# Kernel optimization log

Hardware: AMD Instinct MI355X
Metric: run time of the kernel (lower is better)

## Reference

```python
import jax, jax.numpy as jnp
import numpy as np

N, M, D = 8192, 8192, 512
TINY = jnp.finfo(jnp.float32).tiny


def setup_inputs() -> dict:
    key = jax.random.key(0)
    k1, k2 = jax.random.split(key)
    x = jax.random.normal(k1, (N, D), dtype=jnp.float32)
    x2 = jax.random.normal(k2, (M, D), dtype=jnp.float32)
    # flax self.param with ones initializer (pre-softplus raw params)
    amplitude_raw = jnp.ones((1,), dtype=jnp.float32)
    length_scale_raw = jnp.ones((D,), dtype=jnp.float32)
    return {"x": x, "x2": x2, "amplitude_raw": amplitude_raw,
            "length_scale_raw": length_scale_raw}


def reference(x, x2, amplitude_raw, length_scale_raw):
    # Parameter transforms exactly as in RBFKernelProvider.apply
    amplitude = jax.nn.softplus(amplitude_raw) + TINY          # (1,)
    length_scale = jax.nn.softplus(length_scale_raw) + TINY    # (D,)

    # rbf_kernel_fun: exp(-0.5 * sum(((x - x2)/l)^2)) * amp^2
    # GEMM rewrite of the squared scaled distance (avoids (N,M,D) intermediate):
    # ||xs_i - ys_j||^2 = ||xs_i||^2 + ||ys_j||^2 - 2 xs_i . ys_j
    xs = x / length_scale                                       # (N, D)
    ys = x2 / length_scale                                      # (M, D)
    x_sq = jnp.sum(xs * xs, axis=-1)                            # (N,)
    y_sq = jnp.sum(ys * ys, axis=-1)                            # (M,)
    cross = jnp.einsum('nd,md->nm', xs, ys)                     # (N, M) GEMM
    sq_dists = jnp.maximum(x_sq[:, None] + y_sq[None, :] - 2.0 * cross, 0.0)
    kernel_matrix = jnp.exp(-0.5 * sq_dists)                    # (N, M)
    return (amplitude ** 2) * kernel_matrix
```

## Files before the change

### kernel.cpp

```cpp
#include <hip/hip_runtime.h>

#define AS1 __attribute__((address_space(1)))
#define AS3 __attribute__((address_space(3)))

typedef __attribute__((ext_vector_type(8))) __bf16 bf16x8;
typedef __attribute__((ext_vector_type(4))) float f32x4;

static constexpr int Nn = 8192;
static constexpr int Mm = 8192;
static constexpr int Dd = 512;
static constexpr float TINY = 1.17549435082228751e-38f;

__device__ __forceinline__ float softplus_f(float x) {
    return fmaxf(x, 0.0f) + log1pf(expf(-fabsf(x)));
}

__device__ __forceinline__ unsigned short f2bf(float f) {
    unsigned int u = __float_as_uint(f);
    u = (u + 0x7FFFu + ((u >> 16) & 1u)) >> 16;
    return (unsigned short)u;
}

__device__ __forceinline__ void g2l16(const void* g, void* l) {
    __builtin_amdgcn_global_load_lds((const AS1 unsigned int*)g,
                                     (AS3 unsigned int*)l, 16, 0, 0);
}

__global__ void prep_params(const float* __restrict__ amp_raw,
                            const float* __restrict__ ls_raw,
                            float* __restrict__ inv_l,
                            float* __restrict__ amp2) {
    int t = threadIdx.x;
    if (t < Dd) {
        float l = softplus_f(ls_raw[t]) + TINY;
        inv_l[t] = 1.0f / l;
    }
    if (t == 0) {
        float a = softplus_f(amp_raw[0]) + TINY;
        amp2[0] = a * a;
    }
}

__global__ __launch_bounds__(256) void scale_rows(
        const float* __restrict__ x, const float* __restrict__ x2,
        const float* __restrict__ inv_l,
        unsigned short* __restrict__ xs, unsigned short* __restrict__ ys,
        float* __restrict__ x_sq, float* __restrict__ y_sq) {
    int wave = threadIdx.x >> 6, lane = threadIdx.x & 63;
    int row = blockIdx.x * 4 + wave;

    const float* src; unsigned short* dst; float* nrm; int r;
    if (row < Nn) {
        src = x  + (size_t)row * Dd; dst = xs + (size_t)row * Dd;
        nrm = x_sq + row; r = row;
    } else {
        int m = row - Nn;
        src = x2 + (size_t)m * Dd;   dst = ys + (size_t)m * Dd;
        nrm = y_sq + m; r = m;
    }

    float4 v0 = ((const float4*)src)[lane * 2];
    float4 v1 = ((const float4*)src)[lane * 2 + 1];
    float4 l0 = ((const float4*)inv_l)[lane * 2];
    float4 l1 = ((const float4*)inv_l)[lane * 2 + 1];

    float s[8] = { v0.x*l0.x, v0.y*l0.y, v0.z*l0.z, v0.w*l0.w,
                   v1.x*l1.x, v1.y*l1.y, v1.z*l1.z, v1.w*l1.w };
    float sum = 0.0f;
    unsigned short h[8];
#pragma unroll
    for (int i = 0; i < 8; ++i) { sum += s[i] * s[i]; h[i] = f2bf(s[i]); }

    int g = (r >> 1) & 3;
    int chunk = (lane & ~3) | ((lane & 3) ^ g);
    int4 pk;
    pk.x = (int)h[0] | ((int)h[1] << 16);
    pk.y = (int)h[2] | ((int)h[3] << 16);
    pk.z = (int)h[4] | ((int)h[5] << 16);
    pk.w = (int)h[6] | ((int)h[7] << 16);
    *(int4*)(dst + (size_t)chunk * 8) = pk;

#pragma unroll
    for (int off = 32; off > 0; off >>= 1) sum += __shfl_down(sum, off, 64);
    if (lane == 0) *nrm = sum;
}

__global__ __launch_bounds__(256) void gemm_rbf(
        const unsigned short* __restrict__ xs,
        const unsigned short* __restrict__ ys,
        const float* __restrict__ x_sq, const float* __restrict__ y_sq,
        const float* __restrict__ amp2p, float* __restrict__ out) {

    __shared__ unsigned short sA[128 * 32];
    __shared__ unsigned short sB[128 * 32];

    const int tid  = threadIdx.x;
    const int wave = tid >> 6, lane = tid & 63;
    const int wy = wave >> 1, wx = wave & 1;
    const int lane15 = lane & 15, quad = lane >> 4;
    const int rA  = lane >> 2;
    const int c16 = lane & 3;

    const size_t rowBase = (size_t)blockIdx.y * 128;
    const size_t colBase = (size_t)blockIdx.x * 128;

    f32x4 acc[4][4] = {};
    const int gsw = (lane15 >> 1) & 3;

    for (int kt = 0; kt < 16; ++kt) {
        __syncthreads();
        const size_t kByte = (size_t)kt * 64;
#pragma unroll
        for (int t = 0; t < 2; ++t) {
            int issue = wave * 2 + t;
            int ldsRow = issue * 16 + rA;
            const char* ga = (const char*)(xs + (rowBase + ldsRow) * Dd)
                             + kByte + c16 * 16;
            g2l16(ga, sA + issue * 512);
            const char* gb = (const char*)(ys + (colBase + ldsRow) * Dd)
                             + kByte + c16 * 16;
            g2l16(gb, sB + issue * 512);
        }
        __syncthreads();

        bf16x8 aF[4], bF[4];
#pragma unroll
        for (int ty = 0; ty < 4; ++ty) {
            int rr = wy * 64 + ty * 16 + lane15;
            aF[ty] = *(const bf16x8*)(sA + rr * 32 + ((quad ^ gsw) * 8));
        }
#pragma unroll
        for (int tx = 0; tx < 4; ++tx) {
            int rr = wx * 64 + tx * 16 + lane15;
            bF[tx] = *(const bf16x8*)(sB + rr * 32 + ((quad ^ gsw) * 8));
        }
#pragma unroll
        for (int ty = 0; ty < 4; ++ty)
#pragma unroll
            for (int tx = 0; tx < 4; ++tx)
                acc[ty][tx] = __builtin_amdgcn_mfma_f32_16x16x32_bf16(
                    aF[ty], bF[tx], acc[ty][tx], 0, 0, 0);
    }

    const float amp2 = *amp2p;
#pragma unroll
    for (int ty = 0; ty < 4; ++ty) {
        const size_t r0 = rowBase + wy * 64 + ty * 16 + quad * 4;
        float xq[4];
#pragma unroll
        for (int i = 0; i < 4; ++i) xq[i] = x_sq[r0 + i];
#pragma unroll
        for (int tx = 0; tx < 4; ++tx) {
            const size_t gc = colBase + wx * 64 + tx * 16 + lane15;
            const float yq = y_sq[gc];
            float* o = out + r0 * (size_t)Mm + gc;
#pragma unroll
            for (int reg = 0; reg < 4; ++reg) {
                float sq = fmaxf(xq[reg] + yq - 2.0f * acc[ty][tx][reg], 0.0f);
                o[(size_t)reg * Mm] = amp2 * __expf(-0.5f * sq);
            }
        }
    }
}

__global__ __launch_bounds__(256) void rbf_fallback(
        const float* __restrict__ x, const float* __restrict__ x2,
        const float* __restrict__ amp_raw, const float* __restrict__ ls_raw,
        float* __restrict__ out) {
    __shared__ float il[Dd];
    __shared__ float sX[16 * Dd];
    __shared__ float sY[16 * Dd];
    int tid = threadIdx.x;
    for (int i = tid; i < Dd; i += 256)
        il[i] = 1.0f / (softplus_f(ls_raw[i]) + TINY);
    __syncthreads();
    int bR = blockIdx.y * 16, bC = blockIdx.x * 16;
    for (int i = tid; i < 16 * Dd; i += 256) {
        int r = i >> 9, c = i & (Dd - 1);
        sX[i] = x [(size_t)(bR + r) * Dd + c] * il[c];
        sY[i] = x2[(size_t)(bC + r) * Dd + c] * il[c];
    }
    __syncthreads();
    float a = softplus_f(amp_raw[0]) + TINY;
    float amp2 = a * a;
    int r = tid >> 4, c = tid & 15;
    float sq = 0.0f;
    for (int d = 0; d < Dd; ++d) {
        float df = sX[r * Dd + d] - sY[c * Dd + d];
        sq += df * df;
    }
    out[(size_t)(bR + r) * Mm + (bC + c)] = amp2 * __expf(-0.5f * sq);
}

extern "C" void kernel_launch(void* const* d_in, const int* in_sizes, int n_in,
                              void* d_out, int out_size, void* d_ws, size_t ws_size,
                              hipStream_t stream) {
    const float* x       = (const float*)d_in[0];
    const float* x2      = (const float*)d_in[1];
    const float* amp_raw = (const float*)d_in[2];
    const float* ls_raw  = (const float*)d_in[3];
    float* out = (float*)d_out;

    const size_t OFF_INVL = 0;
    const size_t OFF_AMP2 = 2048;
    const size_t OFF_XSQ  = 4096;
    const size_t OFF_YSQ  = OFF_XSQ + 8192 * 4;
    const size_t OFF_XS   = OFF_YSQ + 8192 * 4;
    const size_t OFF_YS   = OFF_XS + (size_t)Nn * Dd * 2;
    const size_t NEED     = OFF_YS + (size_t)Mm * Dd * 2;

    if (ws_size < NEED) {
        dim3 g(Mm / 16, Nn / 16);
        rbf_fallback<<<g, 256, 0, stream>>>(x, x2, amp_raw, ls_raw, out);
        return;
    }

    char* ws = (char*)d_ws;
    float* inv_l = (float*)(ws + OFF_INVL);
    float* amp2  = (float*)(ws + OFF_AMP2);
    float* x_sq  = (float*)(ws + OFF_XSQ);
    float* y_sq  = (float*)(ws + OFF_YSQ);
    unsigned short* xs = (unsigned short*)(ws + OFF_XS);
    unsigned short* ys = (unsigned short*)(ws + OFF_YS);

    prep_params<<<1, 512, 0, stream>>>(amp_raw, ls_raw, inv_l, amp2);
    scale_rows<<<(Nn + Mm) / 4, 256, 0, stream>>>(x, x2, inv_l, xs, ys, x_sq, y_sq);
    dim3 g(Mm / 128, Nn / 128);
    gemm_rbf<<<g, 256, 0, stream>>>(xs, ys, x_sq, y_sq, amp2, out);
}
```

Measured before the change: 352.5 us.

## Use 32x32 MFMA with deeper K tiles, grouped tile order, and fused param prep

Switches the GEMM from 16x16x32 to 32x32x16 bf16 MFMA with a BK=64 LDS tile and an 8-way XOR swizzle that matches the new staging layout written by scale_rows. It also remaps the 1D grid so blocks are visited in bands, for better L2 reuse of the A/B panels. The prep_params kernel is removed: the softplus parameter transforms are recomputed inside scale_rows and gemm_rbf, which saves one launch. The cost is redundant transcendental work per thread and a larger LDS footprint, though the GEMM is still single-buffered. The kernel is dominated by writing the 256MB output, so gains may be limited.

Measured after the change: 372.8 us. 1.06x slower.

```diff
diff --git a/kernel.cpp b/kernel.cpp
--- a/kernel.cpp
+++ b/kernel.cpp
@@ -4,7 +4,7 @@
 #define AS3 __attribute__((address_space(3)))
 
 typedef __attribute__((ext_vector_type(8))) __bf16 bf16x8;
-typedef __attribute__((ext_vector_type(4))) float f32x4;
+typedef __attribute__((ext_vector_type(16))) float f32x16;
 
 static constexpr int Nn = 8192;
 static constexpr int Mm = 8192;
@@ -26,24 +26,9 @@
                                      (AS3 unsigned int*)l, 16, 0, 0);
 }
 
-__global__ void prep_params(const float* __restrict__ amp_raw,
-                            const float* __restrict__ ls_raw,
-                            float* __restrict__ inv_l,
-                            float* __restrict__ amp2) {
-    int t = threadIdx.x;
-    if (t < Dd) {
-        float l = softplus_f(ls_raw[t]) + TINY;
-        inv_l[t] = 1.0f / l;
-    }
-    if (t == 0) {
-        float a = softplus_f(amp_raw[0]) + TINY;
-        amp2[0] = a * a;
-    }
-}
-
 __global__ __launch_bounds__(256) void scale_rows(
         const float* __restrict__ x, const float* __restrict__ x2,
-        const float* __restrict__ inv_l,
+        const float* __restrict__ ls_raw,
         unsigned short* __restrict__ xs, unsigned short* __restrict__ ys,
         float* __restrict__ x_sq, float* __restrict__ y_sq) {
     int wave = threadIdx.x >> 6, lane = threadIdx.x & 63;
@@ -61,18 +46,22 @@
 
     float4 v0 = ((const float4*)src)[lane * 2];
     float4 v1 = ((const float4*)src)[lane * 2 + 1];
-    float4 l0 = ((const float4*)inv_l)[lane * 2];
-    float4 l1 = ((const float4*)inv_l)[lane * 2 + 1];
-
-    float s[8] = { v0.x*l0.x, v0.y*l0.y, v0.z*l0.z, v0.w*l0.w,
-                   v1.x*l1.x, v1.y*l1.y, v1.z*l1.z, v1.w*l1.w };
+    float4 L0 = ((const float4*)ls_raw)[lane * 2];
+    float4 L1 = ((const float4*)ls_raw)[lane * 2 + 1];
+
+    float il[8] = {
+        1.0f / (softplus_f(L0.x) + TINY), 1.0f / (softplus_f(L0.y) + TINY),
+        1.0f / (softplus_f(L0.z) + TINY), 1.0f / (softplus_f(L0.w) + TINY),
+        1.0f / (softplus_f(L1.x) + TINY), 1.0f / (softplus_f(L1.y) + TINY),
+        1.0f / (softplus_f(L1.z) + TINY), 1.0f / (softplus_f(L1.w) + TINY) };
+    float s[8] = { v0.x*il[0], v0.y*il[1], v0.z*il[2], v0.w*il[3],
+                   v1.x*il[4], v1.y*il[5], v1.z*il[6], v1.w*il[7] };
     float sum = 0.0f;
     unsigned short h[8];
 #pragma unroll
     for (int i = 0; i < 8; ++i) { sum += s[i] * s[i]; h[i] = f2bf(s[i]); }
 
-    int g = (r >> 1) & 3;
-    int chunk = (lane & ~3) | ((lane & 3) ^ g);
+    int chunk = (lane & ~7) | ((lane & 7) ^ (r & 7));
     int4 pk;
     pk.x = (int)h[0] | ((int)h[1] << 16);
     pk.y = (int)h[2] | ((int)h[3] << 16);
@@ -89,76 +78,90 @@
         const unsigned short* __restrict__ xs,
         const unsigned short* __restrict__ ys,
         const float* __restrict__ x_sq, const float* __restrict__ y_sq,
-        const float* __restrict__ amp2p, float* __restrict__ out) {
-
-    __shared__ unsigned short sA[128 * 32];
-    __shared__ unsigned short sB[128 * 32];
+        const float* __restrict__ amp_raw, float* __restrict__ out) {
+
+    __shared__ unsigned short sA[128 * 64];
+    __shared__ unsigned short sB[128 * 64];
 
     const int tid  = threadIdx.x;
     const int wave = tid >> 6, lane = tid & 63;
     const int wy = wave >> 1, wx = wave & 1;
-    const int lane15 = lane & 15, quad = lane >> 4;
-    const int rA  = lane >> 2;
-    const int c16 = lane & 3;
-
-    const size_t rowBase = (size_t)blockIdx.y * 128;
-    const size_t colBase = (size_t)blockIdx.x * 128;
-
-    f32x4 acc[4][4] = {};
-    const int gsw = (lane15 >> 1) & 3;
-
-    for (int kt = 0; kt < 16; ++kt) {
+    const int l31 = lane & 31, half = lane >> 5;
+    const int sr  = lane >> 3, sc = lane & 7;
+
+    const int bid   = blockIdx.x;
+    const int band  = bid & 7;
+    const int kk    = bid >> 3;
+    const int tileY = band * 8 + (kk & 7);
+    const int tileX = kk >> 3;
+    const size_t rowBase = (size_t)tileY * 128;
+    const size_t colBase = (size_t)tileX * 128;
+
+    f32x16 acc[2][2] = {};
+
+    for (int kt = 0; kt < 8; ++kt) {
         __syncthreads();
-        const size_t kByte = (size_t)kt * 64;
-#pragma unroll
-        for (int t = 0; t < 2; ++t) {
-            int issue = wave * 2 + t;
-            int ldsRow = issue * 16 + rA;
-            const char* ga = (const char*)(xs + (rowBase + ldsRow) * Dd)
-                             + kByte + c16 * 16;
+        const size_t kByte = (size_t)kt * 128;
+#pragma unroll
+        for (int t = 0; t < 4; ++t) {
+            int issue = wave * 4 + t;
+            int rowInTile = issue * 8 + sr;
+            const char* ga = (const char*)(xs + (rowBase + rowInTile) * Dd)
+                             + kByte + sc * 16;
             g2l16(ga, sA + issue * 512);
-            const char* gb = (const char*)(ys + (colBase + ldsRow) * Dd)
-                             + kByte + c16 * 16;
+            const char* gb = (const char*)(ys + (colBase + rowInTile) * Dd)
+                             + kByte + sc * 16;
             g2l16(gb, sB + issue * 512);
         }
         __syncthreads();
 
-        bf16x8 aF[4], bF[4];
-#pragma unroll
-        for (int ty = 0; ty < 4; ++ty) {
-            int rr = wy * 64 + ty * 16 + lane15;
-            aF[ty] = *(const bf16x8*)(sA + rr * 32 + ((quad ^ gsw) * 8));
+#pragma unroll
+        for (int ks = 0; ks < 4; ++ks) {
+            bf16x8 aF[2], bF[2];
+#pragma unroll
+            for (int ty = 0; ty < 2; ++ty) {
+                int rr = wy * 64 + ty * 32 + l31;
+                int slot = (ks * 2 + half) ^ (rr & 7);
+                aF[ty] = *(const bf16x8*)(sA + rr * 64 + slot * 8);
+            }
+#pragma unroll
+            for (int tx = 0; tx < 2; ++tx) {
+                int rr = wx * 64 + tx * 32 + l31;
+                int slot = (ks * 2 + half) ^ (rr & 7);
+                bF[tx] = *(const bf16x8*)(sB + rr * 64 + slot * 8);
+            }
+#pragma unroll
+            for (int ty = 0; ty < 2; ++ty)
+#pragma unroll
+                for (int tx = 0; tx < 2; ++tx)
+                    acc[ty][tx] = __builtin_amdgcn_mfma_f32_32x32x16_bf16(
+                        aF[ty], bF[tx], acc[ty][tx], 0, 0, 0);
         }
-#pragma unroll
-        for (int tx = 0; tx < 4; ++tx) {
-            int rr = wx * 64 + tx * 16 + lane15;
-            bF[tx] = *(const bf16x8*)(sB + rr * 32 + ((quad ^ gsw) * 8));
-        }
-#pragma unroll
-        for (int ty = 0; ty < 4; ++ty)
-#pragma unroll
-            for (int tx = 0; tx < 4; ++tx)
-                acc[ty][tx] = __builtin_amdgcn_mfma_f32_16x16x32_bf16(
-                    aF[ty], bF[tx], acc[ty][tx], 0, 0, 0);
-    }
-
-    const float amp2 = *amp2p;
-#pragma unroll
-    for (int ty = 0; ty < 4; ++ty) {
-        const size_t r0 = rowBase + wy * 64 + ty * 16 + quad * 4;
-        float xq[4];
-#pragma unroll
-        for (int i = 0; i < 4; ++i) xq[i] = x_sq[r0 + i];
-#pragma unroll
-        for (int tx = 0; tx < 4; ++tx) {
-            const size_t gc = colBase + wx * 64 + tx * 16 + lane15;
+    }
+
+    float a = softplus_f(amp_raw[0]) + TINY;
+    const float amp2 = a * a;
+#pragma unroll
+    for (int ty = 0; ty < 2; ++ty) {
+        const size_t r0 = rowBase + wy * 64 + ty * 32 + half * 4;
+        float xq[16];
+#pragma unroll
+        for (int g = 0; g < 4; ++g)
+#pragma unroll
+            for (int i = 0; i < 4; ++i) xq[g * 4 + i] = x_sq[r0 + g * 8 + i];
+#pragma unroll
+        for (int tx = 0; tx < 2; ++tx) {
+            const size_t gc = colBase + wx * 64 + tx * 32 + l31;
             const float yq = y_sq[gc];
-            float* o = out + r0 * (size_t)Mm + gc;
-#pragma unroll
-            for (int reg = 0; reg < 4; ++reg) {
-                float sq = fmaxf(xq[reg] + yq - 2.0f * acc[ty][tx][reg], 0.0f);
-                o[(size_t)reg * Mm] = amp2 * __expf(-0.5f * sq);
-            }
+#pragma unroll
+            for (int g = 0; g < 4; ++g)
+#pragma unroll
+                for (int i = 0; i < 4; ++i) {
+                    int reg = g * 4 + i;
+                    float sq = fmaxf(xq[reg] + yq - 2.0f * acc[ty][tx][reg], 0.0f);
+                    out[(r0 + g * 8 + i) * (size_t)Mm + gc] =
+                        amp2 * __expf(-0.5f * sq);
+                }
         }
     }
 }
@@ -201,13 +204,11 @@
     const float* ls_raw  = (const float*)d_in[3];
     float* out = (float*)d_out;
 
-    const size_t OFF_INVL = 0;
-    const size_t OFF_AMP2 = 2048;
-    const size_t OFF_XSQ  = 4096;
-    const size_t OFF_YSQ  = OFF_XSQ + 8192 * 4;
-    const size_t OFF_XS   = OFF_YSQ + 8192 * 4;
-    const size_t OFF_YS   = OFF_XS + (size_t)Nn * Dd * 2;
-    const size_t NEED     = OFF_YS + (size_t)Mm * Dd * 2;
+    const size_t OFF_XSQ = 0;
+    const size_t OFF_YSQ = OFF_XSQ + 8192 * 4;
+    const size_t OFF_XS  = OFF_YSQ + 8192 * 4;
+    const size_t OFF_YS  = OFF_XS + (size_t)Nn * Dd * 2;
+    const size_t NEED    = OFF_YS + (size_t)Mm * Dd * 2;
 
     if (ws_size < NEED) {
         dim3 g(Mm / 16, Nn / 16);
@@ -216,15 +217,12 @@
     }
 
     char* ws = (char*)d_ws;
-    float* inv_l = (float*)(ws + OFF_INVL);
-    float* amp2  = (float*)(ws + OFF_AMP2);
-    float* x_sq  = (float*)(ws + OFF_XSQ);
-    float* y_sq  = (float*)(ws + OFF_YSQ);
+    float* x_sq = (float*)(ws + OFF_XSQ);
+    float* y_sq = (float*)(ws + OFF_YSQ);
     unsigned short* xs = (unsigned short*)(ws + OFF_XS);
     unsigned short* ys = (unsigned short*)(ws + OFF_YS);
 
-    prep_params<<<1, 512, 0, stream>>>(amp_raw, ls_raw, inv_l, amp2);
-    scale_rows<<<(Nn + Mm) / 4, 256, 0, stream>>>(x, x2, inv_l, xs, ys, x_sq, y_sq);
-    dim3 g(Mm / 128, Nn / 128);
-    gemm_rbf<<<g, 256, 0, stream>>>(xs, ys, x_sq, y_sq, amp2, out);
-}
+    scale_rows<<<(Nn + Mm) / 4, 256, 0, stream>>>(x, x2, ls_raw, xs, ys, x_sq, y_sq);
+    gemm_rbf<<<(Nn / 128) * (Mm / 128), 256, 0, stream>>>(
+        xs, ys, x_sq, y_sq, amp_raw, out);
+}
```

## Quantize scaled rows to FP8 and use FP8 MFMA for the cross-term GEMM

Applied to the files above, without the earlier changes.

Converts the length-scaled rows to FP8 (e4m3) instead of bf16 and switches the GEMM to the fp8 16x16x32 MFMA. This halves the global and LDS traffic per K element and halves the K loop iterations. The separate parameter-prep kernel is removed: the softplus and reciprocal are recomputed inline in scale_rows and in gemm_rbf. FP8 cuts precision in the cross term, and because the squared distance is a difference of large terms, this risks accuracy loss.

After: 353.8 us. About the same (+0.4%).

```diff
diff --git a/kernel.cpp b/kernel.cpp
--- a/kernel.cpp
+++ b/kernel.cpp
@@ -3,7 +3,6 @@
 #define AS1 __attribute__((address_space(1)))
 #define AS3 __attribute__((address_space(3)))
 
-typedef __attribute__((ext_vector_type(8))) __bf16 bf16x8;
 typedef __attribute__((ext_vector_type(4))) float f32x4;
 
 static constexpr int Nn = 8192;
@@ -15,70 +14,53 @@
     return fmaxf(x, 0.0f) + log1pf(expf(-fabsf(x)));
 }
 
-__device__ __forceinline__ unsigned short f2bf(float f) {
-    unsigned int u = __float_as_uint(f);
-    u = (u + 0x7FFFu + ((u >> 16) & 1u)) >> 16;
-    return (unsigned short)u;
-}
-
 __device__ __forceinline__ void g2l16(const void* g, void* l) {
     __builtin_amdgcn_global_load_lds((const AS1 unsigned int*)g,
                                      (AS3 unsigned int*)l, 16, 0, 0);
 }
 
-__global__ void prep_params(const float* __restrict__ amp_raw,
-                            const float* __restrict__ ls_raw,
-                            float* __restrict__ inv_l,
-                            float* __restrict__ amp2) {
-    int t = threadIdx.x;
-    if (t < Dd) {
-        float l = softplus_f(ls_raw[t]) + TINY;
-        inv_l[t] = 1.0f / l;
-    }
-    if (t == 0) {
-        float a = softplus_f(amp_raw[0]) + TINY;
-        amp2[0] = a * a;
-    }
-}
-
 __global__ __launch_bounds__(256) void scale_rows(
         const float* __restrict__ x, const float* __restrict__ x2,
-        const float* __restrict__ inv_l,
-        unsigned short* __restrict__ xs, unsigned short* __restrict__ ys,
+        const float* __restrict__ ls_raw,
+        unsigned char* __restrict__ xs, unsigned char* __restrict__ ys,
         float* __restrict__ x_sq, float* __restrict__ y_sq) {
     int wave = threadIdx.x >> 6, lane = threadIdx.x & 63;
     int row = blockIdx.x * 4 + wave;
 
-    const float* src; unsigned short* dst; float* nrm; int r;
+    const float* src; unsigned char* dst; float* nrm; int r;
     if (row < Nn) {
-        src = x  + (size_t)row * Dd; dst = xs + (size_t)row * Dd;
+        src = x  + (size_t)row * Dd; dst = xs + (size_t)row * 512;
         nrm = x_sq + row; r = row;
     } else {
         int m = row - Nn;
-        src = x2 + (size_t)m * Dd;   dst = ys + (size_t)m * Dd;
+        src = x2 + (size_t)m * Dd;   dst = ys + (size_t)m * 512;
         nrm = y_sq + m; r = m;
     }
 
     float4 v0 = ((const float4*)src)[lane * 2];
     float4 v1 = ((const float4*)src)[lane * 2 + 1];
-    float4 l0 = ((const float4*)inv_l)[lane * 2];
-    float4 l1 = ((const float4*)inv_l)[lane * 2 + 1];
-
-    float s[8] = { v0.x*l0.x, v0.y*l0.y, v0.z*l0.z, v0.w*l0.w,
-                   v1.x*l1.x, v1.y*l1.y, v1.z*l1.z, v1.w*l1.w };
+    float4 L0 = ((const float4*)ls_raw)[lane * 2];
+    float4 L1 = ((const float4*)ls_raw)[lane * 2 + 1];
+
+    float il[8] = {
+        1.0f / (softplus_f(L0.x) + TINY), 1.0f / (softplus_f(L0.y) + TINY),
+        1.0f / (softplus_f(L0.z) + TINY), 1.0f / (softplus_f(L0.w) + TINY),
+        1.0f / (softplus_f(L1.x) + TINY), 1.0f / (softplus_f(L1.y) + TINY),
+        1.0f / (softplus_f(L1.z) + TINY), 1.0f / (softplus_f(L1.w) + TINY) };
+    float s[8] = { v0.x*il[0], v0.y*il[1], v0.z*il[2], v0.w*il[3],
+                   v1.x*il[4], v1.y*il[5], v1.z*il[6], v1.w*il[7] };
     float sum = 0.0f;
-    unsigned short h[8];
-#pragma unroll
-    for (int i = 0; i < 8; ++i) { sum += s[i] * s[i]; h[i] = f2bf(s[i]); }
-
-    int g = (r >> 1) & 3;
-    int chunk = (lane & ~3) | ((lane & 3) ^ g);
-    int4 pk;
-    pk.x = (int)h[0] | ((int)h[1] << 16);
-    pk.y = (int)h[2] | ((int)h[3] << 16);
-    pk.z = (int)h[4] | ((int)h[5] << 16);
-    pk.w = (int)h[6] | ((int)h[7] << 16);
-    *(int4*)(dst + (size_t)chunk * 8) = pk;
+#pragma unroll
+    for (int i = 0; i < 8; ++i) sum += s[i] * s[i];
+
+    int p0 = __builtin_amdgcn_cvt_pk_fp8_f32(s[0], s[1], 0, false);
+    p0     = __builtin_amdgcn_cvt_pk_fp8_f32(s[2], s[3], p0, true);
+    int p1 = __builtin_amdgcn_cvt_pk_fp8_f32(s[4], s[5], 0, false);
+    p1     = __builtin_amdgcn_cvt_pk_fp8_f32(s[6], s[7], p1, true);
+
+    int j    = lane >> 1;
+    int phys = (j & ~3) | ((j & 3) ^ (r & 3));
+    *(int2*)(dst + phys * 16 + (lane & 1) * 8) = make_int2(p0, p1);
 
 #pragma unroll
     for (int off = 32; off > 0; off >>= 1) sum += __shfl_down(sum, off, 64);
@@ -86,63 +68,69 @@
 }
 
 __global__ __launch_bounds__(256) void gemm_rbf(
-        const unsigned short* __restrict__ xs,
-        const unsigned short* __restrict__ ys,
+        const unsigned char* __restrict__ xs,
+        const unsigned char* __restrict__ ys,
         const float* __restrict__ x_sq, const float* __restrict__ y_sq,
-        const float* __restrict__ amp2p, float* __restrict__ out) {
-
-    __shared__ unsigned short sA[128 * 32];
-    __shared__ unsigned short sB[128 * 32];
+        const float* __restrict__ amp_raw, float* __restrict__ out) {
+
+    __shared__ unsigned char sA[128 * 64];
+    __shared__ unsigned char sB[128 * 64];
 
     const int tid  = threadIdx.x;
     const int wave = tid >> 6, lane = tid & 63;
     const int wy = wave >> 1, wx = wave & 1;
     const int lane15 = lane & 15, quad = lane >> 4;
-    const int rA  = lane >> 2;
-    const int c16 = lane & 3;
+    const int srow = lane >> 2, schunk = lane & 3;
 
     const size_t rowBase = (size_t)blockIdx.y * 128;
     const size_t colBase = (size_t)blockIdx.x * 128;
 
     f32x4 acc[4][4] = {};
-    const int gsw = (lane15 >> 1) & 3;
-
-    for (int kt = 0; kt < 16; ++kt) {
+
+    for (int kt = 0; kt < 8; ++kt) {
         __syncthreads();
-        const size_t kByte = (size_t)kt * 64;
+        const size_t kOff = (size_t)kt * 64;
 #pragma unroll
         for (int t = 0; t < 2; ++t) {
             int issue = wave * 2 + t;
-            int ldsRow = issue * 16 + rA;
-            const char* ga = (const char*)(xs + (rowBase + ldsRow) * Dd)
-                             + kByte + c16 * 16;
-            g2l16(ga, sA + issue * 512);
-            const char* gb = (const char*)(ys + (colBase + ldsRow) * Dd)
-                             + kByte + c16 * 16;
-            g2l16(gb, sB + issue * 512);
+            int rit = issue * 16 + srow;
+            const unsigned char* ga =
+                xs + (rowBase + rit) * 512 + kOff + schunk * 16;
+            g2l16(ga, sA + issue * 1024);
+            const unsigned char* gb =
+                ys + (colBase + rit) * 512 + kOff + schunk * 16;
+            g2l16(gb, sB + issue * 1024);
         }
         __syncthreads();
 
-        bf16x8 aF[4], bF[4];
-#pragma unroll
-        for (int ty = 0; ty < 4; ++ty) {
-            int rr = wy * 64 + ty * 16 + lane15;
-            aF[ty] = *(const bf16x8*)(sA + rr * 32 + ((quad ^ gsw) * 8));
+#pragma unroll
+        for (int ks = 0; ks < 2; ++ks) {
+            long long aF[4], bF[4];
+#pragma unroll
+            for (int ty = 0; ty < 4; ++ty) {
+                int rr = wy * 64 + ty * 16 + lane15;
+                int phys = (ks * 2 + (quad >> 1)) ^ (rr & 3);
+                aF[ty] = *(const long long*)(sA + rr * 64 + phys * 16
+                                             + (quad & 1) * 8);
+            }
+#pragma unroll
+            for (int tx = 0; tx < 4; ++tx) {
+                int rr = wx * 64 + tx * 16 + lane15;
+                int phys = (ks * 2 + (quad >> 1)) ^ (rr & 3);
+                bF[tx] = *(const long long*)(sB + rr * 64 + phys * 16
+                                             + (quad & 1) * 8);
+            }
+#pragma unroll
+            for (int ty = 0; ty < 4; ++ty)
+#pragma unroll
+                for (int tx = 0; tx < 4; ++tx)
+                    acc[ty][tx] = __builtin_amdgcn_mfma_f32_16x16x32_fp8_fp8(
+                        aF[ty], bF[tx], acc[ty][tx], 0, 0, 0);
         }
-#pragma unroll
-        for (int tx = 0; tx < 4; ++tx) {
-            int rr = wx * 64 + tx * 16 + lane15;
-            bF[tx] = *(const bf16x8*)(sB + rr * 32 + ((quad ^ gsw) * 8));
-        }
-#pragma unroll
-        for (int ty = 0; ty < 4; ++ty)
-#pragma unroll
-            for (int tx = 0; tx < 4; ++tx)
-                acc[ty][tx] = __builtin_amdgcn_mfma_f32_16x16x32_bf16(
-                    aF[ty], bF[tx], acc[ty][tx], 0, 0, 0);
-    }
-
-    const float amp2 = *amp2p;
+    }
+
+    float a = softplus_f(amp_raw[0]) + TINY;
+    const float amp2 = a * a;
 #pragma unroll
     for (int ty = 0; ty < 4; ++ty) {
         const size_t r0 = rowBase + wy * 64 + ty * 16 + quad * 4;
@@ -201,13 +189,11 @@
     const float* ls_raw  = (const float*)d_in[3];
     float* out = (float*)d_out;
 
-    const size_t OFF_INVL = 0;
-    const size_t OFF_AMP2 = 2048;
-    const size_t OFF_XSQ  = 4096;
-    const size_t OFF_YSQ  = OFF_XSQ + 8192 * 4;
-    const size_t OFF_XS   = OFF_YSQ + 8192 * 4;
-    const size_t OFF_YS   = OFF_XS + (size_t)Nn * Dd * 2;
-    const size_t NEED     = OFF_YS + (size_t)Mm * Dd * 2;
+    const size_t OFF_XSQ = 0;
+    const size_t OFF_YSQ = OFF_XSQ + 8192 * 4;
+    const size_t OFF_XS  = OFF_YSQ + 8192 * 4;
+    const size_t OFF_YS  = OFF_XS + (size_t)Nn * Dd;
+    const size_t NEED    = OFF_YS + (size_t)Mm * Dd;
 
     if (ws_size < NEED) {
         dim3 g(Mm / 16, Nn / 16);
@@ -216,15 +202,12 @@
     }
 
     char* ws = (char*)d_ws;
-    float* inv_l = (float*)(ws + OFF_INVL);
-    float* amp2  = (float*)(ws + OFF_AMP2);
-    float* x_sq  = (float*)(ws + OFF_XSQ);
-    float* y_sq  = (float*)(ws + OFF_YSQ);
-    unsigned short* xs = (unsigned short*)(ws + OFF_XS);
-    unsigned short* ys = (unsigned short*)(ws + OFF_YS);
-
-    prep_params<<<1, 512, 0, stream>>>(amp_raw, ls_raw, inv_l, amp2);
-    scale_rows<<<(Nn + Mm) / 4, 256, 0, stream>>>(x, x2, inv_l, xs, ys, x_sq, y_sq);
+    float* x_sq = (float*)(ws + OFF_XSQ);
+    float* y_sq = (float*)(ws + OFF_YSQ);
+    unsigned char* xs = (unsigned char*)(ws + OFF_XS);
+    unsigned char* ys = (unsigned char*)(ws + OFF_YS);
+
+    scale_rows<<<(Nn + Mm) / 4, 256, 0, stream>>>(x, x2, ls_raw, xs, ys, x_sq, y_sq);
     dim3 g(Mm / 128, Nn / 128);
-    gemm_rbf<<<g, 256, 0, stream>>>(xs, ys, x_sq, y_sq, amp2, out);
-}
+    gemm_rbf<<<g, 256, 0, stream>>>(xs, ys, x_sq, y_sq, amp_raw, out);
+}
```
